# Kernel optimization log

Hardware: AMD Instinct MI355X
Metric: run time of the kernel (lower is better)

The kernel has to match this reference:

```python
import jax, jax.numpy as jnp
import numpy as np

COST_CLASS = 1.0
COST_L1 = 1.0


def _lsa(cost):
    """Exact rectangular linear sum assignment (Jonker-Volgenant / e-maxx Hungarian).
    cost: (n, m) numpy float64 with n <= m. Returns ans[n]: column assigned to each row.
    """
    n, m = cost.shape
    INF = np.inf
    u = np.zeros(n + 1)
    v = np.zeros(m + 1)
    p = np.zeros(m + 1, dtype=np.int64)    # p[j]: 1-indexed row matched to column j (0 = free)
    way = np.zeros(m + 1, dtype=np.int64)
    for i in range(1, n + 1):
        p[0] = i
        j0 = 0
        minv = np.full(m + 1, INF)
        used = np.zeros(m + 1, dtype=bool)
        while True:
            used[j0] = True
            i0 = p[j0]
            minv1 = minv[1:]               # view, in-place updates propagate
            jmask = ~used[1:]
            cur = cost[i0 - 1, :] - u[i0] - v[1:]
            upd = jmask & (cur < minv1)
            minv1[upd] = cur[upd]
            way[1:][upd] = j0
            idx = np.nonzero(jmask)[0]
            j1rel = idx[np.argmin(minv1[idx])]
            delta = minv1[j1rel]
            u[p[used]] += delta
            v[used] -= delta
            minv1[jmask] -= delta
            j0 = j1rel + 1
            if p[j0] == 0:
                break
        # augment along the alternating path
        while j0:
            j1 = way[j0]
            p[j0] = p[j1]
            j0 = j1
    ans = np.zeros(n, dtype=np.int64)
    for j in range(1, m + 1):
        if p[j] > 0:
            ans[p[j] - 1] = j - 1
    return ans


def _solve_blocks(blocks):
    """blocks: (B, Q, T) numpy. Per-batch optimal assignment, scipy-compatible output:
    row_ind sorted ascending, min(Q,T) pairs (here Q >= T so T pairs)."""
    blocks = np.asarray(blocks, dtype=np.float64)
    B, Q, T = blocks.shape
    rows = np.empty((B, T), dtype=np.int32)
    cols = np.empty((B, T), dtype=np.int32)
    for b in range(B):
        c = blocks[b]
        if Q >= T:
            ans = _lsa(c.T)                      # ans[t] = matched query q
            order = np.argsort(ans, kind="stable")
            rows[b] = ans[order]
            cols[b] = order
        else:
            ans = _lsa(c)
            rows[b] = np.arange(Q)
            cols[b] = ans
    return rows, cols


def _cost_blocks(outputs, targets):
    """Diagonal (per-sample) blocks of the DETR cost matrix.
    outputs: (B, Q, 1+P); targets: (B, T, 1+P). Returns (B, Q, T).
    Math identical to building the full (B*Q, B*T) matrix and slicing, as in the source."""
    out_prob = jax.nn.softmax(outputs[:, :, 0], axis=-1)      # softmax over the QUERY axis (as in source)
    out_pos = outputs[:, :, 1:]                                # (B, Q, P)
    tgt_pos = targets[:, :, 1:]                                # (B, T, P)
    cost_l1 = jnp.abs(out_pos[:, :, None, :] - tgt_pos[:, None, :, :]).sum(-1)  # L1 cdist, (B, Q, T)
    return COST_CLASS * (-out_prob[:, :, None]) + COST_L1 * cost_l1


def setup_inputs() -> dict:
    key = jax.random.key(0)
    k1, k2 = jax.random.split(key)
    outputs = jax.random.normal(k1, (8, 2048, 3), dtype=jnp.float32)
    targets = jax.random.uniform(k2, (8, 256, 3), dtype=jnp.float32)
    return {"outputs": outputs, "targets": targets}


def reference(outputs, targets):
    blocks = _cost_blocks(outputs, targets)                    # (B, Q, T)
    B, Q, T = blocks.shape
    n = min(Q, T)
    shapes = (jax.ShapeDtypeStruct((B, n), jnp.int32),
              jax.ShapeDtypeStruct((B, n), jnp.int32))
    row_ind, col_ind = jax.pure_callback(_solve_blocks, shapes, blocks)
    return row_ind, col_ind
```

## Files before the change

kernel.cpp:

```cpp
#include <hip/hip_runtime.h>


constexpr int B = 8;
constexpr int Q = 2048;
constexpr int T = 256;
constexpr int NT = 256;
constexpr int KPT = Q / NT;
constexpr int NW = NT / 64;

struct __align__(16) CD { double u; float tx, ty; };

__device__ __forceinline__ unsigned wave_min_u32_dpp(unsigned a) {
  int v = (int)a, t;
  t = __builtin_amdgcn_update_dpp(v, v, 0x111, 0xf, 0xf, false);
  v = ((unsigned)t < (unsigned)v) ? t : v;
  t = __builtin_amdgcn_update_dpp(v, v, 0x112, 0xf, 0xf, false);
  v = ((unsigned)t < (unsigned)v) ? t : v;
  t = __builtin_amdgcn_update_dpp(v, v, 0x114, 0xf, 0xf, false);
  v = ((unsigned)t < (unsigned)v) ? t : v;
  t = __builtin_amdgcn_update_dpp(v, v, 0x118, 0xf, 0xf, false);
  v = ((unsigned)t < (unsigned)v) ? t : v;
  t = __builtin_amdgcn_update_dpp(v, v, 0x142, 0xf, 0xf, false);
  v = ((unsigned)t < (unsigned)v) ? t : v;
  t = __builtin_amdgcn_update_dpp(v, v, 0x143, 0xf, 0xf, false);
  v = ((unsigned)t < (unsigned)v) ? t : v;
  return (unsigned)__builtin_amdgcn_readlane(v, 63);
}

__launch_bounds__(NT, 1)
__global__ void hungarian_r15(const float* __restrict__ outs,
                              const float* __restrict__ tgts,
                              int* __restrict__ out) {
  const int b = blockIdx.x;
  const int tid = threadIdx.x;
  const int lane = tid & 63;
  const int wv = tid >> 6;

  __shared__ CD colDat[Q + 1];
  __shared__ float2 rowTgt[T + 1];
  __shared__ short p[Q + 1];
  __shared__ uint4 pk2[2][NW][2];
  __shared__ double vdelta[Q];
  __shared__ int ansArr[T];
  __shared__ double s_rv[NW];
  __shared__ float sh_f;

  const size_t qbase = (size_t)b * Q;
  const size_t tbase = (size_t)b * T;

  float xs[KPT], qx[KPT], qy[KPT];
#pragma unroll
  for (int k = 0; k < KPT; ++k) {
    const size_t o = (qbase + tid + k * NT) * 3;
    xs[k] = outs[o];
    qx[k] = outs[o + 1];
    qy[k] = outs[o + 2];
  }
  {
    const size_t o = (tbase + tid) * 3;
    rowTgt[tid + 1] = make_float2(tgts[o + 1], tgts[o + 2]);
    if (tid == 0) rowTgt[0] = make_float2(0.f, 0.f);
  }

  float lmax = xs[0];
#pragma unroll
  for (int k = 1; k < KPT; ++k) lmax = fmaxf(lmax, xs[k]);
  for (int off = 32; off > 0; off >>= 1) lmax = fmaxf(lmax, __shfl_down(lmax, off));
  if ((tid & 63) == 0) s_rv[tid >> 6] = (double)lmax;
  __syncthreads();
  if (tid == 0) {
    float m2 = (float)s_rv[0];
    for (int w = 1; w < NW; ++w) m2 = fmaxf(m2, (float)s_rv[w]);
    sh_f = m2;
  }
  __syncthreads();
  const float smax = sh_f;
  float ex[KPT];
  float lsum = 0.f;
#pragma unroll
  for (int k = 0; k < KPT; ++k) { ex[k] = expf(xs[k] - smax); lsum += ex[k]; }
  for (int off = 32; off > 0; off >>= 1) lsum += __shfl_down(lsum, off);
  if ((tid & 63) == 0) s_rv[tid >> 6] = (double)lsum;
  __syncthreads();
  if (tid == 0) {
    float s2 = 0.f;
    for (int w = 0; w < NW; ++w) s2 += (float)s_rv[w];
    sh_f = s2;
  }
  __syncthreads();
  const float ssum = sh_f;
  float np_[KPT];
#pragma unroll
  for (int k = 0; k < KPT; ++k) np_[k] = -(ex[k] / ssum);

  for (int j = tid; j <= Q; j += NT) {
    p[j] = 0;
    CD c0; c0.u = 0.0; c0.tx = -1.0f; c0.ty = 0.0f;
    colDat[j] = c0;
  }
  double vreg[KPT];
#pragma unroll
  for (int k = 0; k < KPT; ++k) {
    vreg[k] = 0.0;
    vdelta[tid + (k << 8)] = 0.0;
  }
  __syncthreads();

  const float FINF = __int_as_float(0x7f800000);
  float2 nxtT = rowTgt[1];
  int par = 0;

  for (int i = 1; i <= T; ++i) {
    unsigned usedMask = 0;
    double D = 0.0;
    int i0 = i;
    double ui0 = 0.0;
    float tX = nxtT.x, tY = nxtT.y;
    int s = 0, S;
    int j1v = 0;
    int recRow = 0, recCol = 0, recPrev = 0;
    double recU = 0.0, recD = 0.0;
    float recTX = 0.f, recTY = 0.f;

    for (;;) {
      const int cpar = par; par ^= 1;

      if (tid == s) {
        recRow = i0; recU = ui0; recTX = tX; recTY = tY; recD = D; recPrev = j1v;
      }

      double cv[KPT];
#pragma unroll
      for (int k = 0; k < KPT; ++k) {
        float cf = fabsf(qx[k] - tX) + fabsf(qy[k] - tY) + np_[k];
        if (usedMask & (1u << k)) cf = FINF;
        cv[k] = ((double)cf - ui0) - vreg[k];
      }
      const double m01 = fmin(cv[0], cv[1]), m23 = fmin(cv[2], cv[3]);
      const double m45 = fmin(cv[4], cv[5]), m67 = fmin(cv[6], cv[7]);
      const double m03 = fmin(m01, m23), m47 = fmin(m45, m67);
      double bval = fmin(m03, m47);
      unsigned emsk = 0;
#pragma unroll
      for (int k = 0; k < KPT; ++k) emsk |= (cv[k] == bval) ? (1u << k) : 0u;
      const int bk = (int)__builtin_ctz(emsk);
      int bidx = 1 + tid + (bk << 8);

      const CD myCd = colDat[bidx];

      bval += 0.0;
      const long long bb = __double_as_longlong(bval);
      const unsigned long long key = (unsigned long long)bb ^
          ((bb < 0) ? 0xFFFFFFFFFFFFFFFFull : 0x8000000000000000ull);
      const unsigned khi = (unsigned)(key >> 32);
      const unsigned klo = (unsigned)key;

      const unsigned minhi = wave_min_u32_dpp(khi);
      const unsigned long long mask = __ballot(khi == minhi);
      int wl;
      if (__popcll(mask) == 1) {
        wl = (int)__ffsll(mask) - 1;
      } else {
        unsigned wklo = 0xffffffffu; int widx = 0x7fffffff; wl = 0;
        unsigned long long mm = mask;
        while (mm) {
          const int l = (int)__ffsll(mm) - 1; mm &= mm - 1;
          const unsigned lo2 = (unsigned)__builtin_amdgcn_readlane((int)klo, l);
          const int ix2 = __builtin_amdgcn_readlane(bidx, l);
          if (lo2 < wklo || (lo2 == wklo && ix2 < widx)) {
            wklo = lo2; widx = ix2; wl = l;
          }
        }
      }
      if (lane == wl) {
        pk2[cpar][wv][0] = make_uint4(minhi, klo, (unsigned)bidx, 0u);
        const unsigned long long cu =
            (unsigned long long)__double_as_longlong(myCd.u);
        pk2[cpar][wv][1] = make_uint4((unsigned)cu, (unsigned)(cu >> 32),
                                      __float_as_uint(myCd.tx),
                                      __float_as_uint(myCd.ty));
      }
      __syncthreads();

      const uint4 c0v = pk2[cpar][0][0];
      const uint4 c1v = pk2[cpar][1][0];
      const uint4 c2v = pk2[cpar][2][0];
      const uint4 c3v = pk2[cpar][3][0];
      const uint4 d0v = pk2[cpar][0][1];
      const uint4 d1v = pk2[cpar][1][1];
      const uint4 d2v = pk2[cpar][2][1];
      const uint4 d3v = pk2[cpar][3][1];

      const unsigned long long k0b = ((unsigned long long)c0v.x << 32) | c0v.y;
      const unsigned long long k1b = ((unsigned long long)c1v.x << 32) | c1v.y;
      const unsigned long long k2b = ((unsigned long long)c2v.x << 32) | c2v.y;
      const unsigned long long k3b = ((unsigned long long)c3v.x << 32) | c3v.y;
      const int j0b = (int)c0v.z, j1bb = (int)c1v.z;
      const int j2b = (int)c2v.z, j3b = (int)c3v.z;
      const bool w01 = (k1b < k0b) || (k1b == k0b && j1bb < j0b);
      const unsigned long long k01 = w01 ? k1b : k0b;
      const int j01 = w01 ? j1bb : j0b;
      const bool w23 = (k3b < k2b) || (k3b == k2b && j3b < j2b);
      const unsigned long long k23 = w23 ? k3b : k2b;
      const int j23 = w23 ? j3b : j2b;
      const bool wf = (k23 < k01) || (k23 == k01 && j23 < j01);
      const unsigned long long bkk = wf ? k23 : k01;
      const int j1 = wf ? j23 : j01;
      const unsigned ulA = w01 ? d1v.x : d0v.x, uhA = w01 ? d1v.y : d0v.y;
      const unsigned xAf = w01 ? d1v.z : d0v.z, yAf = w01 ? d1v.w : d0v.w;
      const unsigned ulB = w23 ? d3v.x : d2v.x, uhB = w23 ? d3v.y : d2v.y;
      const unsigned xBf = w23 ? d3v.z : d2v.z, yBf = w23 ? d3v.w : d2v.w;
      const unsigned ulW = wf ? ulB : ulA, uhW = wf ? uhB : uhA;
      const unsigned xW = wf ? xBf : xAf, yW = wf ? yBf : yAf;
      const double cdun = __longlong_as_double(
          (long long)(((unsigned long long)uhW << 32) | ulW));
      const float cdtx = __uint_as_float(xW);
      const float cdty = __uint_as_float(yW);

      const long long db = (long long)((bkk & 0x8000000000000000ull)
                                           ? (bkk ^ 0x8000000000000000ull) : ~bkk);
      D += __longlong_as_double(db);
      if (tid == ((j1 - 1) & 255)) usedMask |= 1u << ((j1 - 1) >> 8);
      if (tid == s) recCol = j1;
      const int pj1 = (int)p[j1];
      j1v = j1;
      ++s;
      if (cdtx < 0.0f) { S = s; break; }
      ui0 = cdun; tX = cdtx; tY = cdty; i0 = pj1;
    }

    nxtT = rowTgt[i < T ? i + 1 : T];
    if (S == 1) {
      const int c = j1v - 1;
      if (tid == (c & 255)) {
        p[j1v] = (short)i;
        CD c2; c2.u = D; c2.tx = tX; c2.ty = tY;
        colDat[j1v] = c2;
      }
    } else {
      const double Dfin = D;
      if (tid < S) {
        p[recCol] = (short)recRow;
        const double unew = recU + (Dfin - recD);
        CD c2; c2.u = unew; c2.tx = recTX; c2.ty = recTY;
        colDat[recCol] = c2;
        if (tid >= 1) {
          vdelta[recPrev - 1] = Dfin - recD;
        }
      }
      __syncthreads();
#pragma unroll
      for (int k = 0; k < KPT; ++k) {
        const double dv = vdelta[tid + (k << 8)];
        vreg[k] -= dv;
        vdelta[tid + (k << 8)] = 0.0;
      }
    }
  }
  __syncthreads();

  for (int j = 1 + tid; j <= Q; j += NT) {
    const int pi = (int)p[j];
    if (pi > 0) ansArr[pi - 1] = j - 1;
  }
  __syncthreads();
  const int a = ansArr[tid];
  int rank = 0;
  for (int t2 = 0; t2 < T; ++t2) rank += (ansArr[t2] < a) ? 1 : 0;
  out[(size_t)b * T + rank] = a;
  out[(size_t)B * T + (size_t)b * T + rank] = tid;
}

extern "C" void kernel_launch(void* const* d_in, const int* in_sizes, int n_in,
                              void* d_out, int out_size, void* d_ws, size_t ws_size,
                              hipStream_t stream) {
  const float* outs = (const float*)d_in[0];
  const float* tgts = (const float*)d_in[1];
  int* out = (int*)d_out;
  hungarian_r15<<<B, NT, 0, stream>>>(outs, tgts, out);
}
```

Measured before the change: 861.5 us.

## Double threads per block to 512 with four columns per thread in Hungarian kernel

Raises the block size from 256 to 512 threads so each thread owns 4 query columns instead of 8. This reworks the column-to-thread mapping, the used-mask ownership test and the cross-wave reduction, which now merges 8 wave candidates instead of 4. The softmax is computed by the first 256 threads only. Each step of the serial augmenting-path loop does less per-thread work, but the block barrier now spans 8 waves and the final reduction is longer.

Measured after the change: 1.300 ms. 1.51x slower.

```diff
diff --git a/kernel.cpp b/kernel.cpp
--- a/kernel.cpp
+++ b/kernel.cpp
@@ -4,8 +4,8 @@
 constexpr int B = 8;
 constexpr int Q = 2048;
 constexpr int T = 256;
-constexpr int NT = 256;
-constexpr int KPT = Q / NT;
+constexpr int NT = 512;
+constexpr int KPT = 4;
 constexpr int NW = NT / 64;
 
 struct __align__(16) CD { double u; float tx, ty; };
@@ -28,13 +28,15 @@
 }
 
 __launch_bounds__(NT, 1)
-__global__ void hungarian_r15(const float* __restrict__ outs,
+__global__ void hungarian_r18(const float* __restrict__ outs,
                               const float* __restrict__ tgts,
                               int* __restrict__ out) {
   const int b = blockIdx.x;
   const int tid = threadIdx.x;
   const int lane = tid & 63;
   const int wv = tid >> 6;
+  const int half = tid >> 8;
+  const int base = tid & 255;
 
   __shared__ CD colDat[Q + 1];
   __shared__ float2 rowTgt[T + 1];
@@ -42,56 +44,65 @@
   __shared__ uint4 pk2[2][NW][2];
   __shared__ double vdelta[Q];
   __shared__ int ansArr[T];
-  __shared__ double s_rv[NW];
+  __shared__ double s_rv[4];
   __shared__ float sh_f;
 
   const size_t qbase = (size_t)b * Q;
   const size_t tbase = (size_t)b * T;
 
-  float xs[KPT], qx[KPT], qy[KPT];
+  float xsm[KPT], qx[KPT], qy[KPT];
 #pragma unroll
   for (int k = 0; k < KPT; ++k) {
-    const size_t o = (qbase + tid + k * NT) * 3;
-    xs[k] = outs[o];
+    const int c = base + ((half * 4 + k) << 8);
+    const size_t o = (qbase + c) * 3;
+    xsm[k] = outs[o];
     qx[k] = outs[o + 1];
     qy[k] = outs[o + 2];
   }
-  {
+  float xs8[8];
+  if (tid < 256) {
+#pragma unroll
+    for (int k = 0; k < 8; ++k) xs8[k] = outs[(qbase + base + (k << 8)) * 3];
+  }
+  if (tid < 256) {
     const size_t o = (tbase + tid) * 3;
     rowTgt[tid + 1] = make_float2(tgts[o + 1], tgts[o + 2]);
     if (tid == 0) rowTgt[0] = make_float2(0.f, 0.f);
   }
 
-  float lmax = xs[0];
-#pragma unroll
-  for (int k = 1; k < KPT; ++k) lmax = fmaxf(lmax, xs[k]);
-  for (int off = 32; off > 0; off >>= 1) lmax = fmaxf(lmax, __shfl_down(lmax, off));
-  if ((tid & 63) == 0) s_rv[tid >> 6] = (double)lmax;
+  if (tid < 256) {
+    float lmax = xs8[0];
+#pragma unroll
+    for (int k = 1; k < 8; ++k) lmax = fmaxf(lmax, xs8[k]);
+    for (int off = 32; off > 0; off >>= 1) lmax = fmaxf(lmax, __shfl_down(lmax, off));
+    if ((tid & 63) == 0) s_rv[tid >> 6] = (double)lmax;
+  }
   __syncthreads();
   if (tid == 0) {
     float m2 = (float)s_rv[0];
-    for (int w = 1; w < NW; ++w) m2 = fmaxf(m2, (float)s_rv[w]);
+    for (int w = 1; w < 4; ++w) m2 = fmaxf(m2, (float)s_rv[w]);
     sh_f = m2;
   }
   __syncthreads();
   const float smax = sh_f;
-  float ex[KPT];
-  float lsum = 0.f;
-#pragma unroll
-  for (int k = 0; k < KPT; ++k) { ex[k] = expf(xs[k] - smax); lsum += ex[k]; }
-  for (int off = 32; off > 0; off >>= 1) lsum += __shfl_down(lsum, off);
-  if ((tid & 63) == 0) s_rv[tid >> 6] = (double)lsum;
+  if (tid < 256) {
+    float lsum = 0.f;
+#pragma unroll
+    for (int k = 0; k < 8; ++k) lsum += expf(xs8[k] - smax);
+    for (int off = 32; off > 0; off >>= 1) lsum += __shfl_down(lsum, off);
+    if ((tid & 63) == 0) s_rv[tid >> 6] = (double)lsum;
+  }
   __syncthreads();
   if (tid == 0) {
     float s2 = 0.f;
-    for (int w = 0; w < NW; ++w) s2 += (float)s_rv[w];
+    for (int w = 0; w < 4; ++w) s2 += (float)s_rv[w];
     sh_f = s2;
   }
   __syncthreads();
   const float ssum = sh_f;
   float np_[KPT];
 #pragma unroll
-  for (int k = 0; k < KPT; ++k) np_[k] = -(ex[k] / ssum);
+  for (int k = 0; k < KPT; ++k) np_[k] = -(expf(xsm[k] - smax) / ssum);
 
   for (int j = tid; j <= Q; j += NT) {
     p[j] = 0;
@@ -102,7 +113,7 @@
 #pragma unroll
   for (int k = 0; k < KPT; ++k) {
     vreg[k] = 0.0;
-    vdelta[tid + (k << 8)] = 0.0;
+    vdelta[base + ((half * 4 + k) << 8)] = 0.0;
   }
   __syncthreads();
 
@@ -137,14 +148,12 @@
         cv[k] = ((double)cf - ui0) - vreg[k];
       }
       const double m01 = fmin(cv[0], cv[1]), m23 = fmin(cv[2], cv[3]);
-      const double m45 = fmin(cv[4], cv[5]), m67 = fmin(cv[6], cv[7]);
-      const double m03 = fmin(m01, m23), m47 = fmin(m45, m67);
-      double bval = fmin(m03, m47);
+      double bval = fmin(m01, m23);
       unsigned emsk = 0;
 #pragma unroll
       for (int k = 0; k < KPT; ++k) emsk |= (cv[k] == bval) ? (1u << k) : 0u;
       const int bk = (int)__builtin_ctz(emsk);
-      int bidx = 1 + tid + (bk << 8);
+      int bidx = 1 + base + ((half * 4 + bk) << 8);
 
       const CD myCd = colDat[bidx];
 
@@ -182,45 +191,48 @@
       }
       __syncthreads();
 
-      const uint4 c0v = pk2[cpar][0][0];
-      const uint4 c1v = pk2[cpar][1][0];
-      const uint4 c2v = pk2[cpar][2][0];
-      const uint4 c3v = pk2[cpar][3][0];
-      const uint4 d0v = pk2[cpar][0][1];
-      const uint4 d1v = pk2[cpar][1][1];
-      const uint4 d2v = pk2[cpar][2][1];
-      const uint4 d3v = pk2[cpar][3][1];
-
-      const unsigned long long k0b = ((unsigned long long)c0v.x << 32) | c0v.y;
-      const unsigned long long k1b = ((unsigned long long)c1v.x << 32) | c1v.y;
-      const unsigned long long k2b = ((unsigned long long)c2v.x << 32) | c2v.y;
-      const unsigned long long k3b = ((unsigned long long)c3v.x << 32) | c3v.y;
-      const int j0b = (int)c0v.z, j1bb = (int)c1v.z;
-      const int j2b = (int)c2v.z, j3b = (int)c3v.z;
-      const bool w01 = (k1b < k0b) || (k1b == k0b && j1bb < j0b);
-      const unsigned long long k01 = w01 ? k1b : k0b;
-      const int j01 = w01 ? j1bb : j0b;
-      const bool w23 = (k3b < k2b) || (k3b == k2b && j3b < j2b);
-      const unsigned long long k23 = w23 ? k3b : k2b;
-      const int j23 = w23 ? j3b : j2b;
-      const bool wf = (k23 < k01) || (k23 == k01 && j23 < j01);
-      const unsigned long long bkk = wf ? k23 : k01;
-      const int j1 = wf ? j23 : j01;
-      const unsigned ulA = w01 ? d1v.x : d0v.x, uhA = w01 ? d1v.y : d0v.y;
-      const unsigned xAf = w01 ? d1v.z : d0v.z, yAf = w01 ? d1v.w : d0v.w;
-      const unsigned ulB = w23 ? d3v.x : d2v.x, uhB = w23 ? d3v.y : d2v.y;
-      const unsigned xBf = w23 ? d3v.z : d2v.z, yBf = w23 ? d3v.w : d2v.w;
-      const unsigned ulW = wf ? ulB : ulA, uhW = wf ? uhB : uhA;
-      const unsigned xW = wf ? xBf : xAf, yW = wf ? yBf : yAf;
+      unsigned long long kk[NW]; int jj[NW]; uint4 dd[NW];
+#pragma unroll
+      for (int w = 0; w < NW; ++w) {
+        const uint4 cw = pk2[cpar][w][0];
+        dd[w] = pk2[cpar][w][1];
+        kk[w] = ((unsigned long long)cw.x << 32) | cw.y;
+        jj[w] = (int)cw.z;
+      }
+      unsigned long long kA, kB, kC, kD2, kE, kF2, kW;
+      int jA, jB, jC, jD2, jE, jF2, jW;
+      uint4 dA, dB, dC, dD2, dE, dF2, dW;
+      {
+        bool w;
+        w = (kk[1] < kk[0]) || (kk[1] == kk[0] && jj[1] < jj[0]);
+        kA = w ? kk[1] : kk[0]; jA = w ? jj[1] : jj[0]; dA = w ? dd[1] : dd[0];
+        w = (kk[3] < kk[2]) || (kk[3] == kk[2] && jj[3] < jj[2]);
+        kB = w ? kk[3] : kk[2]; jB = w ? jj[3] : jj[2]; dB = w ? dd[3] : dd[2];
+        w = (kk[5] < kk[4]) || (kk[5] == kk[4] && jj[5] < jj[4]);
+        kC = w ? kk[5] : kk[4]; jC = w ? jj[5] : jj[4]; dC = w ? dd[5] : dd[4];
+        w = (kk[7] < kk[6]) || (kk[7] == kk[6] && jj[7] < jj[6]);
+        kD2 = w ? kk[7] : kk[6]; jD2 = w ? jj[7] : jj[6]; dD2 = w ? dd[7] : dd[6];
+        w = (kB < kA) || (kB == kA && jB < jA);
+        kE = w ? kB : kA; jE = w ? jB : jA; dE = w ? dB : dA;
+        w = (kD2 < kC) || (kD2 == kC && jD2 < jC);
+        kF2 = w ? kD2 : kC; jF2 = w ? jD2 : jC; dF2 = w ? dD2 : dC;
+        w = (kF2 < kE) || (kF2 == kE && jF2 < jE);
+        kW = w ? kF2 : kE; jW = w ? jF2 : jE; dW = w ? dF2 : dE;
+      }
+      const int j1 = jW;
       const double cdun = __longlong_as_double(
-          (long long)(((unsigned long long)uhW << 32) | ulW));
-      const float cdtx = __uint_as_float(xW);
-      const float cdty = __uint_as_float(yW);
-
-      const long long db = (long long)((bkk & 0x8000000000000000ull)
-                                           ? (bkk ^ 0x8000000000000000ull) : ~bkk);
+          (long long)(((unsigned long long)dW.y << 32) | dW.x));
+      const float cdtx = __uint_as_float(dW.z);
+      const float cdty = __uint_as_float(dW.w);
+
+      const long long db = (long long)((kW & 0x8000000000000000ull)
+                                           ? (kW ^ 0x8000000000000000ull) : ~kW);
       D += __longlong_as_double(db);
-      if (tid == ((j1 - 1) & 255)) usedMask |= 1u << ((j1 - 1) >> 8);
+      {
+        const int c = j1 - 1;
+        if (tid == ((c & 255) | ((c >> 10) << 8)))
+          usedMask |= 1u << ((c >> 8) & 3);
+      }
       if (tid == s) recCol = j1;
       const int pj1 = (int)p[j1];
       j1v = j1;
@@ -232,7 +244,7 @@
     nxtT = rowTgt[i < T ? i + 1 : T];
     if (S == 1) {
       const int c = j1v - 1;
-      if (tid == (c & 255)) {
+      if (tid == ((c & 255) | ((c >> 10) << 8))) {
         p[j1v] = (short)i;
         CD c2; c2.u = D; c2.tx = tX; c2.ty = tY;
         colDat[j1v] = c2;
@@ -251,9 +263,10 @@
       __syncthreads();
 #pragma unroll
       for (int k = 0; k < KPT; ++k) {
-        const double dv = vdelta[tid + (k << 8)];
+        const int a = base + ((half * 4 + k) << 8);
+        const double dv = vdelta[a];
         vreg[k] -= dv;
-        vdelta[tid + (k << 8)] = 0.0;
+        vdelta[a] = 0.0;
       }
     }
   }
@@ -264,11 +277,13 @@
     if (pi > 0) ansArr[pi - 1] = j - 1;
   }
   __syncthreads();
-  const int a = ansArr[tid];
-  int rank = 0;
-  for (int t2 = 0; t2 < T; ++t2) rank += (ansArr[t2] < a) ? 1 : 0;
-  out[(size_t)b * T + rank] = a;
-  out[(size_t)B * T + (size_t)b * T + rank] = tid;
+  if (tid < T) {
+    const int a = ansArr[tid];
+    int rank = 0;
+    for (int t2 = 0; t2 < T; ++t2) rank += (ansArr[t2] < a) ? 1 : 0;
+    out[(size_t)b * T + rank] = a;
+    out[(size_t)B * T + (size_t)b * T + rank] = tid;
+  }
 }
 
 extern "C" void kernel_launch(void* const* d_in, const int* in_sizes, int n_in,
@@ -277,5 +292,5 @@
   const float* outs = (const float*)d_in[0];
   const float* tgts = (const float*)d_in[1];
   int* out = (int*)d_out;
-  hungarian_r15<<<B, NT, 0, stream>>>(outs, tgts, out);
+  hungarian_r18<<<B, NT, 0, stream>>>(outs, tgts, out);
 }
```
